# Kernel tuning notes

Measured on AMD Instinct MI355X. Metric: run time of the kernel, lower is better.

Reference implementation:

```python
import jax, jax.numpy as jnp
import numpy as np

N = 100000      # num nodes
E = 1600000     # num edges
B = 256         # num graphs in batch
D_IN = 128
H = 256
BN_EPS = 1e-5


def setup_inputs() -> dict:
    key = jax.random.key(0)
    ks = jax.random.split(key, 16)
    inp = {}
    inp["x"] = jax.random.normal(ks[0], (N, D_IN), jnp.float32)
    inp["edge_index"] = jax.random.randint(ks[1], (2, E), 0, N, jnp.int32)
    inp["edge_weight"] = jax.random.uniform(ks[2], (E,), jnp.float32)
    inp["batch"] = jnp.sort(jax.random.randint(ks[3], (N,), 0, B, jnp.int32))
    # GCN layer 1
    inp["W1"] = jax.random.normal(ks[4], (D_IN, H), jnp.float32) * 0.05
    inp["b1"] = jnp.zeros((H,), jnp.float32)
    inp["g1"] = jnp.ones((H,), jnp.float32)
    inp["be1"] = jnp.zeros((H,), jnp.float32)
    inp["rm1"] = jnp.zeros((H,), jnp.float32)
    inp["rv1"] = jnp.ones((H,), jnp.float32)
    # GCN layer 2
    inp["W2"] = jax.random.normal(ks[5], (H, H), jnp.float32) * 0.05
    inp["b2"] = jnp.zeros((H,), jnp.float32)
    inp["g2"] = jnp.ones((H,), jnp.float32)
    inp["be2"] = jnp.zeros((H,), jnp.float32)
    inp["rm2"] = jnp.zeros((H,), jnp.float32)
    inp["rv2"] = jnp.ones((H,), jnp.float32)
    # classifier: Linear(256,256)+BN, Linear(256,128)+BN, Linear(128,2)
    inp["cW1"] = jax.random.normal(ks[6], (H, 256), jnp.float32) * 0.05
    inp["cb1"] = jnp.zeros((256,), jnp.float32)
    inp["cg1"] = jnp.ones((256,), jnp.float32)
    inp["cbe1"] = jnp.zeros((256,), jnp.float32)
    inp["crm1"] = jnp.zeros((256,), jnp.float32)
    inp["crv1"] = jnp.ones((256,), jnp.float32)
    inp["cW2"] = jax.random.normal(ks[7], (256, 128), jnp.float32) * 0.05
    inp["cb2"] = jnp.zeros((128,), jnp.float32)
    inp["cg2"] = jnp.ones((128,), jnp.float32)
    inp["cbe2"] = jnp.zeros((128,), jnp.float32)
    inp["crm2"] = jnp.zeros((128,), jnp.float32)
    inp["crv2"] = jnp.ones((128,), jnp.float32)
    inp["cW3"] = jax.random.normal(ks[8], (128, 2), jnp.float32) * 0.05
    inp["cb3"] = jnp.zeros((2,), jnp.float32)
    return inp


def _bn(x, g, b, rm, rv):
    # eval-mode BatchNorm1d with running stats
    return (x - rm) * jax.lax.rsqrt(rv + BN_EPS) * g + b


def _gcn_conv(x, W, b, src, dst, ew):
    # PyG GCNConv: add self-loops (weight 1), symmetric normalization
    deg = jax.ops.segment_sum(ew, dst, num_segments=N) + 1.0  # incl. self loop
    dinv = jnp.where(deg > 0, jax.lax.rsqrt(deg), 0.0)        # [N]
    h = x @ W                                                  # [N, out]
    norm = dinv[src] * ew * dinv[dst]                          # [E]
    agg = jax.ops.segment_sum(h[src] * norm[:, None], dst, num_segments=N)
    agg = agg + h * (dinv * dinv)[:, None]                     # self-loop term
    return agg + b


def _forward(x, edge_index, edge_weight, batch,
             W1, b1, g1, be1, rm1, rv1,
             W2, b2, g2, be2, rm2, rv2,
             cW1, cb1, cg1, cbe1, crm1, crv1,
             cW2, cb2, cg2, cbe2, crm2, crv2,
             cW3, cb3):
    src, dst = edge_index[0], edge_index[1]
    # layer 0 (no residual: i == 0)
    h = jax.nn.relu(_bn(_gcn_conv(x, W1, b1, src, dst, edge_weight), g1, be1, rm1, rv1))
    res = h
    # layer 1 (residual: dims match, i > 0); dropout = identity (eval)
    h = jax.nn.relu(_bn(_gcn_conv(h, W2, b2, src, dst, edge_weight), g2, be2, rm2, rv2))
    h = h + res
    # global mean pool per graph
    cnt = jax.ops.segment_sum(jnp.ones((N,), x.dtype), batch, num_segments=B)
    emb = jax.ops.segment_sum(h, batch, num_segments=B) / jnp.maximum(cnt, 1.0)[:, None]
    # classifier MLP
    z = jax.nn.relu(_bn(emb @ cW1 + cb1, cg1, cbe1, crm1, crv1))
    z = jax.nn.relu(_bn(z @ cW2 + cb2, cg2, cbe2, crm2, crv2))
    logits = z @ cW3 + cb3
    return logits, emb


def reference(x, edge_index, edge_weight, batch,
              W1, b1, g1, be1, rm1, rv1,
              W2, b2, g2, be2, rm2, rv2,
              cW1, cb1, cg1, cbe1, crm1, crv1,
              cW2, cb2, cg2, cbe2, crm2, crv2,
              cW3, cb3):
    return _forward(x, edge_index, edge_weight, batch,
                    W1, b1, g1, be1, rm1, rv1,
                    W2, b2, g2, be2, rm2, rv2,
                    cW1, cb1, cg1, cbe1, crm1, crv1,
                    cW2, cb2, cg2, cbe2, crm2, crv2,
                    cW3, cb3)
```

## Files before the change

kernel.cpp:

```cpp
#include <hip/hip_runtime.h>
#include <stdint.h>

#define NN 100000
#define NE 1600000
#define NB 256
#define DIN 128
#define HH 256
#define BN_EPS 1e-5f

typedef unsigned short bf16_t;
typedef __attribute__((ext_vector_type(8))) short short8;
typedef __attribute__((ext_vector_type(4))) short short4v;
typedef __attribute__((ext_vector_type(4))) float f32x4;
typedef __attribute__((ext_vector_type(2))) float f32x2;

struct __align__(8) EPair { int c; float v; };

#define DEG_MASK ((1ULL << 40) - 1ULL)
#define DEG_ONE  (1ULL << 40)
#define FXS 1048576.0f

__device__ __forceinline__ float bf2f(unsigned short u) {
    union { unsigned int i; float f; } v;
    v.i = ((unsigned int)u) << 16;
    return v.f;
}
__device__ __forceinline__ bf16_t f2bf(float f) {
    union { float f; unsigned int i; } v;
    v.f = f;
    unsigned int x = v.i;
    return (bf16_t)((x + 0x7fffu + ((x >> 16) & 1u)) >> 16);
}
__device__ __forceinline__ float ldp(const void* b, int i, int f) {
    return f ? ((const float*)b)[i] : bf2f(((const unsigned short*)b)[i]);
}
__device__ __forceinline__ int dflag_from(const void* rv) {
    return ((((const unsigned int*)rv)[0] & 0xffffu) == 0u) ? 1 : 0;
}

__device__ __forceinline__ void fmadd_row8p(f32x2* acc2, uint2 w, float v) {
#if defined(__HIP_DEVICE_COMPILE__)
    f32x2 vv = {v, v};
    acc2[0] += __builtin_amdgcn_cvt_pk_f32_fp8((int)w.x, false) * vv;
    acc2[1] += __builtin_amdgcn_cvt_pk_f32_fp8((int)w.x, true)  * vv;
    acc2[2] += __builtin_amdgcn_cvt_pk_f32_fp8((int)w.y, false) * vv;
    acc2[3] += __builtin_amdgcn_cvt_pk_f32_fp8((int)w.y, true)  * vv;
#else
    (void)acc2; (void)w; (void)v;
#endif
}
__device__ __forceinline__ unsigned char enc_fp8(float v) {
#if defined(__HIP_DEVICE_COMPILE__)
    int pk = __builtin_amdgcn_cvt_pk_fp8_f32(v, v, 0, false);
    return (unsigned char)(pk & 0xff);
#else
    (void)v; return 0;
#endif
}
__device__ __forceinline__ unsigned int pack4_fp8(float a, float b, float c, float d) {
#if defined(__HIP_DEVICE_COMPILE__)
    int w = __builtin_amdgcn_cvt_pk_fp8_f32(a, b, 0, false);
    w = __builtin_amdgcn_cvt_pk_fp8_f32(c, d, w, true);
    return (unsigned int)w;
#else
    (void)a; (void)b; (void)c; (void)d; return 0;
#endif
}

__device__ __forceinline__ void pack_one(const void* __restrict__ W, bf16_t* __restrict__ P,
                                         int S, int idx, int f) {
    int lane = idx & 63;
    int ts = idx >> 6;
    int s = ts % S;
    int t = ts / S;
    int q = lane >> 4, m = lane & 15;
    int colbase = t * 16 + m;
    int krow = 32 * s + 8 * q;
#pragma unroll
    for (int j = 0; j < 8; j++) P[idx * 8 + j] = f2bf(ldp(W, (krow + j) * 256 + colbase, f));
}

__global__ __launch_bounds__(256) void prep_kernel(const void* __restrict__ x, unsigned int* __restrict__ xc8,
                                                   const void* __restrict__ ew,
                                                   const int* __restrict__ dst,
                                                   const int* __restrict__ batch,
                                                   unsigned long long* __restrict__ cd8,
                                                   unsigned char* __restrict__ occ,
                                                   int* __restrict__ gcount,
                                                   const void* __restrict__ W1, bf16_t* __restrict__ P1,
                                                   const void* __restrict__ W2, bf16_t* __restrict__ P2,
                                                   const void* __restrict__ rv) {
    int i = blockIdx.x * blockDim.x + threadIdx.x;
    int stride = gridDim.x * blockDim.x;
    int shard = blockIdx.x & 7;
    int f = dflag_from(rv);
    if (i < 12288) {
        if (i < 4096) pack_one(W1, P1, 4, i, f);
        else          pack_one(W2, P2, 8, i - 4096, f);
    }
    if (f) {
        const float4* xs = (const float4*)x;
        for (int j = i; j < NN * DIN / 4; j += stride) {
            float4 w = xs[j];
            xc8[j] = pack4_fp8(w.x, w.y, w.z, w.w);
        }
    } else {
        const uint2* xs = (const uint2*)x;
        for (int j = i; j < NN * DIN / 4; j += stride) {
            uint2 w = xs[j];
            xc8[j] = pack4_fp8(bf2f((unsigned short)(w.x & 0xffffu)), bf2f((unsigned short)(w.x >> 16)),
                               bf2f((unsigned short)(w.y & 0xffffu)), bf2f((unsigned short)(w.y >> 16)));
        }
    }
    for (int j = i; j < NE; j += stride) {
        float w = ldp(ew, j, f);
        int d = dst[j];
        unsigned long long wfx = (unsigned long long)(unsigned int)(w * FXS + 0.5f);
        unsigned long long old = atomicAdd(&cd8[(size_t)shard * NN + d], DEG_ONE | wfx);
        occ[j] = (unsigned char)(old >> 40);
    }
    int lane = threadIdx.x & 63;
    for (int j = i; j < NN; j += stride) {
        int b = batch[j];
        bool boundary = (lane == 0) || (j == 0) || (batch[j - 1] != b);
        unsigned long long bmask = __ballot(boundary);
        bool islast = (lane == 63) || (j + 1 >= NN) || (batch[j + 1] != b);
        if (islast) {
            unsigned long long below = bmask & ((lane == 63) ? ~0ull : ((1ull << (lane + 1)) - 1ull));
            int first = 63 - __builtin_clzll(below);
            atomicAdd(&gcount[b], lane - first + 1);
        }
    }
}

#define SCAN_NB ((NN + 1023) / 1024)

__global__ __launch_bounds__(1024) void scanA(const unsigned long long* __restrict__ cd8,
                                              int* __restrict__ rowptr,
                                              float* __restrict__ dinv,
                                              int* __restrict__ bsum) {
    __shared__ int wsum[16];
    int tid = threadIdx.x, lane = tid & 63, wid = tid >> 6;
    int i = blockIdx.x * 1024 + tid;
    int v = 0;
    if (i < NN) {
        float wf = 0.f;
#pragma unroll
        for (int k = 0; k < 8; k++) {
            unsigned long long cv = cd8[(size_t)k * NN + i];
            v += (int)(cv >> 40);
            wf += (float)(cv & DEG_MASK);
        }
        dinv[i] = rsqrtf(wf * (1.0f / FXS) + 1.0f);
    }
    int sc = v;
#pragma unroll
    for (int off = 1; off < 64; off <<= 1) {
        int t = __shfl_up(sc, off, 64);
        if (lane >= off) sc += t;
    }
    if (lane == 63) wsum[wid] = sc;
    __syncthreads();
    if (wid == 0 && lane < 16) {
        int ws = wsum[lane];
        int scw = ws;
#pragma unroll
        for (int off = 1; off < 16; off <<= 1) {
            int t = __shfl_up(scw, off, 64);
            if (lane >= off) scw += t;
        }
        if (lane == 15) bsum[blockIdx.x] = scw;
        wsum[lane] = scw - ws;
    }
    __syncthreads();
    if (i < NN) rowptr[i] = wsum[wid] + sc - v;
}

__global__ __launch_bounds__(64) void scanB(int* __restrict__ bsum, int* __restrict__ rowptr,
                                            const int* __restrict__ gcount, int* __restrict__ gptr,
                                            EPair* __restrict__ ep) {
    int lane = threadIdx.x;
    EPair pz; pz.c = 0; pz.v = 0.f;
    ep[NE + lane] = pz;
    {
        int i0 = lane * 2;
        int v0 = (i0 < SCAN_NB) ? bsum[i0] : 0;
        int v1 = (i0 + 1 < SCAN_NB) ? bsum[i0 + 1] : 0;
        int tsum = v0 + v1;
        int sc = tsum;
#pragma unroll
        for (int off = 1; off < 64; off <<= 1) {
            int t = __shfl_up(sc, off, 64);
            if (lane >= off) sc += t;
        }
        int excl = sc - tsum;
        if (i0 < SCAN_NB) bsum[i0] = excl;
        if (i0 + 1 < SCAN_NB) bsum[i0 + 1] = excl + v0;
        if (lane == 63) rowptr[NN] = sc;
    }
    {
        int i0 = lane * 4;
        int v0 = gcount[i0], v1 = gcount[i0 + 1], v2 = gcount[i0 + 2], v3 = gcount[i0 + 3];
        int tsum = v0 + v1 + v2 + v3;
        int sc = tsum;
#pragma unroll
        for (int off = 1; off < 64; off <<= 1) {
            int t = __shfl_up(sc, off, 64);
            if (lane >= off) sc += t;
        }
        int excl = sc - tsum;
        gptr[i0] = excl;
        gptr[i0 + 1] = excl + v0;
        gptr[i0 + 2] = excl + v0 + v1;
        gptr[i0 + 3] = excl + v0 + v1 + v2;
        if (lane == 63) gptr[256] = sc;
    }
}

__global__ __launch_bounds__(1024) void scanC(int* __restrict__ rowptr, const int* __restrict__ bsum,
                                              const unsigned long long* __restrict__ cd8,
                                              int* __restrict__ offs) {
    int i = blockIdx.x * 1024 + threadIdx.x;
    if (i < NN) {
        int rp = rowptr[i] + bsum[blockIdx.x];
        rowptr[i] = rp;
        int cum = rp;
#pragma unroll
        for (int k = 0; k < 8; k++) {
            offs[(size_t)k * NN + i] = cum;
            cum += (int)(cd8[(size_t)k * NN + i] >> 40);
        }
    }
}

__global__ __launch_bounds__(256) void scatter_kernel(const int* __restrict__ src,
                                                      const int* __restrict__ dst,
                                                      const void* __restrict__ ew,
                                                      const float* __restrict__ dinv,
                                                      const int* __restrict__ offs,
                                                      const unsigned char* __restrict__ occ,
                                                      EPair* __restrict__ ep,
                                                      const void* __restrict__ rv) {
    int i = blockIdx.x * blockDim.x + threadIdx.x;
    int f = dflag_from(rv);
    int shard = blockIdx.x & 7;
    if (i < NE) {
        int s = src[i], d = dst[i];
        float nv = dinv[s] * ldp(ew, i, f) * dinv[d];
        int pos = offs[(size_t)shard * NN + d] + occ[i];
        EPair pr;
        pr.c = s;
        pr.v = nv;
        ep[pos] = pr;
    }
}

template <int K, bool WRITE_OUT, bool ACCUM>
__global__ __launch_bounds__(256, 6) void fused_layer(
        const void* __restrict__ Xv,
        const bf16_t* __restrict__ P,
        const int* __restrict__ rowptr,
        const EPair* __restrict__ ep,
        const float* __restrict__ dinv,
        const int* __restrict__ batch,
        const void* __restrict__ bias,
        const void* __restrict__ gam,
        const void* __restrict__ bet,
        const void* __restrict__ rmean,
        const void* __restrict__ rvar,
        void* __restrict__ outbuf,
        float* __restrict__ partial,
        float* __restrict__ partial2,
        float* __restrict__ embf) {
    constexpr int S = K / 32;
    constexpr int ROWELL = K + 8;
    constexpr int LPR = K / 8;
    constexpr int EDG = 64 / LPR;
    constexpr int UN = 8;
    constexpr int BE = EDG * UN;
    constexpr int U16 = 16 / EDG;
    constexpr int U32 = 32 / EDG;
    constexpr int SH = (K == 256) ? 8 : 7;
    __shared__ __align__(16) bf16_t T[16 * ROWELL];
    __shared__ EPair WINDOW[4][64];
    const char* Xb = (const char*)Xv;
    int fl = dflag_from(rvar);
    int widx = threadIdx.x >> 6;
    int lane = threadIdx.x & 63;
    int h = lane / LPR;
    int l = lane % LPR;
    int f0 = l * 8;
    unsigned loff = (unsigned)(l * 8);
    int rowbase = blockIdx.x * 16;

    int rp = rowptr[rowbase + (lane < 17 ? lane : 16)];
    float dvv = dinv[rowbase + (lane < 16 ? lane : 15)];

    int j0 = widx * 4;
    EPair win = ep[__shfl(rp, j0) + lane];
    for (int j = 0; j < 4; j++) {
        int r = j0 + j;
        int e0 = __shfl(rp, r);
        int e1 = __shfl(rp, r + 1);
        int n = e1 - e0;
        float di = __shfl(dvv, r);
        int node = rowbase + r;
        EPair nxtwin = ep[e1 + lane];
        f32x2 acc2[4];
#pragma unroll
        for (int c = 0; c < 4; c++) acc2[c] = (f32x2){0.f, 0.f};
        {
            EPair sw;
            bool okl = lane < n;
            sw.c = okl ? win.c : node;
            sw.v = okl ? win.v : 0.f;
            WINDOW[widx][lane] = sw;
        }
        uint2 wself = *(const uint2*)(Xb + ((unsigned)node << SH) + loff);

#define GBATCH(B0, NU) { \
        uint2 wreg[NU]; \
        float vreg[NU]; \
        _Pragma("unroll") \
        for (int u = 0; u < NU; u++) { \
            EPair e = WINDOW[widx][(B0) + EDG * u + h]; \
            vreg[u] = e.v; \
            wreg[u] = *(const uint2*)(Xb + ((unsigned)e.c << SH) + loff); \
        } \
        _Pragma("unroll") \
        for (int u = 0; u < NU; u++) fmadd_row8p(acc2, wreg[u], vreg[u]); \
    }

        if (n <= 16) {
            GBATCH(0, U16)
        } else if (n <= 32) {
            GBATCH(0, U32)
        } else {
            int base = 0;
            while (true) {
                int winend = n - base;
                if (winend > 64) winend = 64;
                for (int s0 = 0; s0 < winend; s0 += BE) {
                    GBATCH(s0, UN)
                }
                base += winend;
                if (base >= n) break;
                EPair nw = ep[e0 + base + lane];
                EPair sw;
                bool okl = (base + lane) < n;
                sw.c = okl ? nw.c : node;
                sw.v = okl ? nw.v : 0.f;
                WINDOW[widx][lane] = sw;
            }
        }
#undef GBATCH
        fmadd_row8p(acc2, wself, (h == 0) ? di * di : 0.f);
        float acc[8];
#pragma unroll
        for (int c = 0; c < 4; c++) { acc[2 * c] = acc2[c][0]; acc[2 * c + 1] = acc2[c][1]; }
#pragma unroll
        for (int d = LPR; d < 64; d <<= 1) {
#pragma unroll
            for (int c = 0; c < 8; c++) acc[c] += __shfl_xor(acc[c], d);
        }
        if (h == 0) {
            short8 o;
#pragma unroll
            for (int c = 0; c < 8; c++) o[c] = (short)f2bf(acc[c]);
            *(short8*)&T[r * ROWELL + f0] = o;
        }
        win = nxtwin;
    }
    __syncthreads();

    int m = lane & 15, q = lane >> 4;
    f32x4 acc16[4];
#pragma unroll
    for (int tt = 0; tt < 4; tt++) acc16[tt] = (f32x4){0.f, 0.f, 0.f, 0.f};
#pragma unroll
    for (int s = 0; s < S; s++) {
        short8 af = *(const short8*)&T[m * ROWELL + 32 * s + 8 * q];
#pragma unroll
        for (int tt = 0; tt < 4; tt++) {
            int t = j0 + tt;
            short8 bfr = *(const short8*)(P + ((size_t)(t * S + s) * 64 + lane) * 8);
            acc16[tt] = __builtin_amdgcn_mfma_f32_16x16x32_bf16(af, bfr, acc16[tt], 0, 0, 0);
        }
    }
    if (WRITE_OUT) __syncthreads();
    unsigned char* T8 = (unsigned char*)T;

    int g0 = batch[rowbase];
    int g15 = batch[rowbase + 15];
    int rg[4];
#pragma unroll
    for (int r = 0; r < 4; r++) rg[r] = batch[rowbase + q * 4 + r];
#pragma unroll
    for (int tt = 0; tt < 4; tt++) {
        int col = (j0 + tt) * 16 + m;
        float a = rsqrtf(ldp(rvar, col, fl) + BN_EPS) * ldp(gam, col, fl);
        float bc = (ldp(bias, col, fl) - ldp(rmean, col, fl)) * a + ldp(bet, col, fl);
        float cs0 = 0.f, cs1 = 0.f;
#pragma unroll
        for (int r = 0; r < 4; r++) {
            int row = q * 4 + r;
            float v = fmaxf(acc16[tt][r] * a + bc, 0.f);
            if (WRITE_OUT) T8[row * 256 + col] = enc_fp8(v);
            if (rg[r] == g0) cs0 += v;
            else if (rg[r] == g15) cs1 += v;
            else atomicAdd(&embf[(size_t)rg[r] * 256 + col], v);
        }
        cs0 += __shfl_xor(cs0, 16, 64);
        cs0 += __shfl_xor(cs0, 32, 64);
        cs1 += __shfl_xor(cs1, 16, 64);
        cs1 += __shfl_xor(cs1, 32, 64);
        if (q == 0) {
            size_t pidx = (size_t)blockIdx.x * 256 + col;
            partial[pidx]  = (ACCUM ? partial[pidx]  : 0.f) + cs0;
            partial2[pidx] = (ACCUM ? partial2[pidx] : 0.f) + cs1;
        }
    }
    if (WRITE_OUT) {
        __syncthreads();
        int tid = threadIdx.x;
        uint4 wv = *(const uint4*)&T8[tid * 16];
        *(uint4*)((char*)outbuf + (size_t)rowbase * 256 + tid * 16) = wv;
    }
}

__global__ __launch_bounds__(256) void classifier_kernel(const float* __restrict__ partial,
                                                         const float* __restrict__ partial2,
                                                         const int* __restrict__ gptr,
                                                         const float* __restrict__ embf,
                                                         const void* cW1, const void* cb1,
                                                         const void* cg1, const void* cbe1,
                                                         const void* crm1, const void* crv1,
                                                         const void* cW2, const void* cb2,
                                                         const void* cg2, const void* cbe2,
                                                         const void* crm2, const void* crv2,
                                                         const void* cW3, const void* cb3,
                                                         void* __restrict__ d_out) {
    int g = blockIdx.x, tid = threadIdx.x;
    int fl = dflag_from(crv1);
    __shared__ float se[256];
    __shared__ float z1[256];
    __shared__ float z2[128];
    int s = gptr[g], e = gptr[g + 1];
    float acc = embf[g * 256 + tid];
    int blo = (s + 15) >> 4, bhi = (e + 15) >> 4;
    for (int b = blo; b < bhi; b++) acc += partial[(size_t)b * 256 + tid];
    int bs = s >> 4;
    if ((s & 15) && (16 * bs + 15) < e) acc += partial2[(size_t)bs * 256 + tid];
    float mval = acc / fmaxf((float)(e - s), 1.f);
    se[tid] = mval;
    if (fl) ((float*)d_out)[512 + g * 256 + tid] = mval;
    else    ((bf16_t*)d_out)[512 + g * 256 + tid] = f2bf(mval);
    __syncthreads();
    {
        float sm = 0.f;
#pragma unroll 8
        for (int k = 0; k < 256; k++) sm += se[k] * ldp(cW1, k * 256 + tid, fl);
        sm += ldp(cb1, tid, fl);
        sm = (sm - ldp(crm1, tid, fl)) * rsqrtf(ldp(crv1, tid, fl) + BN_EPS) * ldp(cg1, tid, fl) + ldp(cbe1, tid, fl);
        z1[tid] = fmaxf(sm, 0.f);
    }
    __syncthreads();
    if (tid < 128) {
        float sm = 0.f;
#pragma unroll 8
        for (int k = 0; k < 256; k++) sm += z1[k] * ldp(cW2, k * 128 + tid, fl);
        sm += ldp(cb2, tid, fl);
        sm = (sm - ldp(crm2, tid, fl)) * rsqrtf(ldp(crv2, tid, fl) + BN_EPS) * ldp(cg2, tid, fl) + ldp(cbe2, tid, fl);
        z2[tid] = fmaxf(sm, 0.f);
    }
    __syncthreads();
    if (tid < 2) {
        float sm = 0.f;
        for (int k = 0; k < 128; k++) sm += z2[k] * ldp(cW3, k * 2 + tid, fl);
        sm += ldp(cb3, tid, fl);
        if (fl) ((float*)d_out)[g * 2 + tid] = sm;
        else    ((bf16_t*)d_out)[g * 2 + tid] = f2bf(sm);
    }
}

extern "C" void kernel_launch(void* const* d_in, const int* in_sizes, int n_in,
                              void* d_out, int out_size, void* d_ws, size_t ws_size,
                              hipStream_t stream) {
    const void* x    = d_in[0];
    const int*  eidx = (const int*)d_in[1];
    const void* ew   = d_in[2];
    const int*  batch= (const int*)d_in[3];
    const void* W1   = d_in[4];
    const void* b1   = d_in[5];
    const void* g1   = d_in[6];
    const void* be1  = d_in[7];
    const void* rm1  = d_in[8];
    const void* rv1  = d_in[9];
    const void* W2   = d_in[10];
    const void* b2   = d_in[11];
    const void* g2   = d_in[12];
    const void* be2  = d_in[13];
    const void* rm2  = d_in[14];
    const void* rv2  = d_in[15];
    const void* cW1  = d_in[16];
    const void* cb1  = d_in[17];
    const void* cg1  = d_in[18];
    const void* cbe1 = d_in[19];
    const void* crm1 = d_in[20];
    const void* crv1 = d_in[21];
    const void* cW2  = d_in[22];
    const void* cb2  = d_in[23];
    const void* cg2  = d_in[24];
    const void* cbe2 = d_in[25];
    const void* crm2 = d_in[26];
    const void* crv2 = d_in[27];
    const void* cW3  = d_in[28];
    const void* cb3  = d_in[29];

    const int* src = eidx;
    const int* dst = eidx + NE;

    char* p = (char*)d_ws;
    auto alloc = [&](size_t bytes) -> void* {
        void* r = (void*)p;
        p += (bytes + 255) & ~(size_t)255;
        return r;
    };
    unsigned long long* cd8 = (unsigned long long*)alloc((size_t)8 * NN * 8);
    int*    gcount = (int*)alloc((size_t)NB * 4);
    float*  embf   = (float*)alloc((size_t)NB * 256 * 4);
    size_t zspan = (char*)p - (char*)cd8;
    int*    rowptr = (int*)alloc((size_t)(NN + 1) * 4);
    float*  dinv   = (float*)alloc((size_t)NN * 4);
    int*    bsum   = (int*)alloc((size_t)SCAN_NB * 4);
    int*    gptr   = (int*)alloc((size_t)(NB + 1) * 4);
    int*    offs   = (int*)alloc((size_t)8 * NN * 4);
    unsigned char* occ = (unsigned char*)alloc((size_t)NE);
    float*  partial = (float*)alloc((size_t)(NN / 16) * 256 * 4);
    float*  partial2= (float*)alloc((size_t)(NN / 16) * 256 * 4);
    EPair*  ep     = (EPair*)alloc((size_t)(NE + 64) * 8);
    unsigned int* xc8 = (unsigned int*)alloc((size_t)NN * DIN);
    bf16_t* pW1    = (bf16_t*)alloc((size_t)DIN * 256 * 2);
    bf16_t* pW2    = (bf16_t*)alloc((size_t)256 * 256 * 2);
    void*   hl     = alloc((size_t)NN * 256);

    (void)hipMemsetAsync(cd8, 0, zspan, stream);

    prep_kernel<<<2048, 256, 0, stream>>>(x, xc8, ew, dst, batch, cd8, occ, gcount,
                                          W1, pW1, W2, pW2, rv1);
    scanA<<<SCAN_NB, 1024, 0, stream>>>(cd8, rowptr, dinv, bsum);
    scanB<<<1, 64, 0, stream>>>(bsum, rowptr, gcount, gptr, ep);
    scanC<<<SCAN_NB, 1024, 0, stream>>>(rowptr, bsum, cd8, offs);
    scatter_kernel<<<NE / 256, 256, 0, stream>>>(src, dst, ew, dinv, offs, occ, ep, rv1);

    int blocks = NN / 16;
    fused_layer<128, true, false><<<blocks, 256, 0, stream>>>(
        xc8, pW1, rowptr, ep, dinv, batch, b1, g1, be1, rm1, rv1, hl, partial, partial2, embf);
    fused_layer<256, false, true><<<blocks, 256, 0, stream>>>(
        hl, pW2, rowptr, ep, dinv, batch, b2, g2, be2, rm2, rv2, nullptr, partial, partial2, embf);

    classifier_kernel<<<NB, 256, 0, stream>>>(partial, partial2, gptr, embf,
                                              cW1, cb1, cg1, cbe1, crm1, crv1,
                                              cW2, cb2, cg2, cbe2, crm2, crv2,
                                              cW3, cb3, d_out);
}
```

Baseline: 487.5 us.

## Software-pipeline neighbor gathers across rows with double-buffered edge windows

When all four rows a wavefront handles have at most 32 edges, the gather phase now issues the feature loads for the next row before accumulating the current one, using two shared-memory edge windows and two register sets. The aim is to hide global gather latency by keeping more loads in flight per wave. The n<=16 special case is dropped, so short rows always do a full 32-edge batch with padding. The launch bound drops from 6 to 4 waves per SIMD to make room for the extra registers, which lowers occupancy.

```diff
diff --git a/kernel.cpp b/kernel.cpp
--- a/kernel.cpp
+++ b/kernel.cpp
@@ -256,7 +256,7 @@
 }
 
 template <int K, bool WRITE_OUT, bool ACCUM>
-__global__ __launch_bounds__(256, 6) void fused_layer(
+__global__ __launch_bounds__(256, 4) void fused_layer(
         const void* __restrict__ Xv,
         const bf16_t* __restrict__ P,
         const int* __restrict__ rowptr,
@@ -278,11 +278,10 @@
     constexpr int EDG = 64 / LPR;
     constexpr int UN = 8;
     constexpr int BE = EDG * UN;
-    constexpr int U16 = 16 / EDG;
     constexpr int U32 = 32 / EDG;
     constexpr int SH = (K == 256) ? 8 : 7;
     __shared__ __align__(16) bf16_t T[16 * ROWELL];
-    __shared__ EPair WINDOW[4][64];
+    __shared__ EPair WIN2[4][2][64];
     const char* Xb = (const char*)Xv;
     int fl = dflag_from(rvar);
     int widx = threadIdx.x >> 6;
@@ -297,51 +296,109 @@
     float dvv = dinv[rowbase + (lane < 16 ? lane : 15)];
 
     int j0 = widx * 4;
-    EPair win = ep[__shfl(rp, j0) + lane];
-    for (int j = 0; j < 4; j++) {
-        int r = j0 + j;
-        int e0 = __shfl(rp, r);
-        int e1 = __shfl(rp, r + 1);
-        int n = e1 - e0;
-        float di = __shfl(dvv, r);
-        int node = rowbase + r;
-        EPair nxtwin = ep[e1 + lane];
-        f32x2 acc2[4];
-#pragma unroll
-        for (int c = 0; c < 4; c++) acc2[c] = (f32x2){0.f, 0.f};
-        {
-            EPair sw;
-            bool okl = lane < n;
-            sw.c = okl ? win.c : node;
-            sw.v = okl ? win.v : 0.f;
-            WINDOW[widx][lane] = sw;
-        }
-        uint2 wself = *(const uint2*)(Xb + ((unsigned)node << SH) + loff);
-
-#define GBATCH(B0, NU) { \
-        uint2 wreg[NU]; \
-        float vreg[NU]; \
+    int e_0 = __shfl(rp, j0),     e_1 = __shfl(rp, j0 + 1);
+    int e_2 = __shfl(rp, j0 + 2), e_3 = __shfl(rp, j0 + 3);
+    int e_4 = __shfl(rp, j0 + 4);
+    int n0 = e_1 - e_0, n1 = e_2 - e_1, n2 = e_3 - e_2, n3 = e_4 - e_3;
+    float di0 = __shfl(dvv, j0),     di1 = __shfl(dvv, j0 + 1);
+    float di2 = __shfl(dvv, j0 + 2), di3 = __shfl(dvv, j0 + 3);
+    int nd0 = rowbase + j0, nd1 = nd0 + 1, nd2 = nd0 + 2, nd3 = nd0 + 3;
+    int nmax = max(max(n0, n1), max(n2, n3));
+    EPair w_next = ep[e_0 + lane];
+
+#define PSTAGE(SL, NV, ND) { \
+        EPair sw_; bool ok_ = lane < (NV); \
+        sw_.c = ok_ ? w_next.c : (ND); \
+        sw_.v = ok_ ? w_next.v : 0.f; \
+        WIN2[widx][SL][lane] = sw_; }
+
+#define PISSUE(WR, WS, SL, ND) { \
         _Pragma("unroll") \
-        for (int u = 0; u < NU; u++) { \
-            EPair e = WINDOW[widx][(B0) + EDG * u + h]; \
-            vreg[u] = e.v; \
-            wreg[u] = *(const uint2*)(Xb + ((unsigned)e.c << SH) + loff); \
+        for (int u = 0; u < U32; u++) { \
+            int c_ = WIN2[widx][SL][EDG * u + h].c; \
+            WR[u] = *(const uint2*)(Xb + ((unsigned)c_ << SH) + loff); \
         } \
+        WS = *(const uint2*)(Xb + ((unsigned)(ND) << SH) + loff); }
+
+#define PCONSUME(WR, WS, SL, DI, RR) { \
+        f32x2 acc2[4]; \
         _Pragma("unroll") \
-        for (int u = 0; u < NU; u++) fmadd_row8p(acc2, wreg[u], vreg[u]); \
-    }
-
-        if (n <= 16) {
-            GBATCH(0, U16)
-        } else if (n <= 32) {
-            GBATCH(0, U32)
-        } else {
+        for (int c_ = 0; c_ < 4; c_++) acc2[c_] = (f32x2){0.f, 0.f}; \
+        _Pragma("unroll") \
+        for (int u = 0; u < U32; u++) { \
+            float v_ = WIN2[widx][SL][EDG * u + h].v; \
+            fmadd_row8p(acc2, WR[u], v_); \
+        } \
+        fmadd_row8p(acc2, WS, (h == 0) ? (DI) * (DI) : 0.f); \
+        float acc[8]; \
+        _Pragma("unroll") \
+        for (int c_ = 0; c_ < 4; c_++) { acc[2 * c_] = acc2[c_][0]; acc[2 * c_ + 1] = acc2[c_][1]; } \
+        _Pragma("unroll") \
+        for (int d_ = LPR; d_ < 64; d_ <<= 1) { \
+            _Pragma("unroll") \
+            for (int c_ = 0; c_ < 8; c_++) acc[c_] += __shfl_xor(acc[c_], d_); \
+        } \
+        if (h == 0) { \
+            short8 o_; \
+            _Pragma("unroll") \
+            for (int c_ = 0; c_ < 8; c_++) o_[c_] = (short)f2bf(acc[c_]); \
+            *(short8*)&T[(RR) * ROWELL + f0] = o_; \
+        } }
+
+    if (nmax <= 32) {
+        uint2 wregA[U32], wregB[U32];
+        uint2 wselfA, wselfB;
+        PSTAGE(0, n0, nd0)
+        w_next = ep[e_1 + lane];
+        PISSUE(wregA, wselfA, 0, nd0)
+        PSTAGE(1, n1, nd1)
+        w_next = ep[e_2 + lane];
+        PISSUE(wregB, wselfB, 1, nd1)
+        PCONSUME(wregA, wselfA, 0, di0, j0 + 0)
+        PSTAGE(0, n2, nd2)
+        w_next = ep[e_3 + lane];
+        PISSUE(wregA, wselfA, 0, nd2)
+        PCONSUME(wregB, wselfB, 1, di1, j0 + 1)
+        PSTAGE(1, n3, nd3)
+        PISSUE(wregB, wselfB, 1, nd3)
+        PCONSUME(wregA, wselfA, 0, di2, j0 + 2)
+        PCONSUME(wregB, wselfB, 1, di3, j0 + 3)
+    } else {
+        EPair win = w_next;
+        for (int j = 0; j < 4; j++) {
+            int r = j0 + j;
+            int e0 = __shfl(rp, r);
+            int e1 = __shfl(rp, r + 1);
+            int n = e1 - e0;
+            float di = __shfl(dvv, r);
+            int node = rowbase + r;
+            EPair nxtwin = ep[e1 + lane];
+            f32x2 acc2[4];
+#pragma unroll
+            for (int c = 0; c < 4; c++) acc2[c] = (f32x2){0.f, 0.f};
+            {
+                EPair sw;
+                bool okl = lane < n;
+                sw.c = okl ? win.c : node;
+                sw.v = okl ? win.v : 0.f;
+                WIN2[widx][0][lane] = sw;
+            }
+            uint2 wself = *(const uint2*)(Xb + ((unsigned)node << SH) + loff);
             int base = 0;
             while (true) {
                 int winend = n - base;
                 if (winend > 64) winend = 64;
                 for (int s0 = 0; s0 < winend; s0 += BE) {
-                    GBATCH(s0, UN)
+                    uint2 wreg[UN];
+                    float vreg[UN];
+#pragma unroll
+                    for (int u = 0; u < UN; u++) {
+                        EPair e = WIN2[widx][0][s0 + EDG * u + h];
+                        vreg[u] = e.v;
+                        wreg[u] = *(const uint2*)(Xb + ((unsigned)e.c << SH) + loff);
+                    }
+#pragma unroll
+                    for (int u = 0; u < UN; u++) fmadd_row8p(acc2, wreg[u], vreg[u]);
                 }
                 base += winend;
                 if (base >= n) break;
@@ -350,27 +407,29 @@
                 bool okl = (base + lane) < n;
                 sw.c = okl ? nw.c : node;
                 sw.v = okl ? nw.v : 0.f;
-                WINDOW[widx][lane] = sw;
+                WIN2[widx][0][lane] = sw;
             }
-        }
-#undef GBATCH
-        fmadd_row8p(acc2, wself, (h == 0) ? di * di : 0.f);
-        float acc[8];
-#pragma unroll
-        for (int c = 0; c < 4; c++) { acc[2 * c] = acc2[c][0]; acc[2 * c + 1] = acc2[c][1]; }
-#pragma unroll
-        for (int d = LPR; d < 64; d <<= 1) {
-#pragma unroll
-            for (int c = 0; c < 8; c++) acc[c] += __shfl_xor(acc[c], d);
-        }
-        if (h == 0) {
-            short8 o;
-#pragma unroll
-            for (int c = 0; c < 8; c++) o[c] = (short)f2bf(acc[c]);
-            *(short8*)&T[r * ROWELL + f0] = o;
-        }
-        win = nxtwin;
-    }
+            fmadd_row8p(acc2, wself, (h == 0) ? di * di : 0.f);
+            float acc[8];
+#pragma unroll
+            for (int c = 0; c < 4; c++) { acc[2 * c] = acc2[c][0]; acc[2 * c + 1] = acc2[c][1]; }
+#pragma unroll
+            for (int d = LPR; d < 64; d <<= 1) {
+#pragma unroll
+                for (int c = 0; c < 8; c++) acc[c] += __shfl_xor(acc[c], d);
+            }
+            if (h == 0) {
+                short8 o;
+#pragma unroll
+                for (int c = 0; c < 8; c++) o[c] = (short)f2bf(acc[c]);
+                *(short8*)&T[r * ROWELL + f0] = o;
+            }
+            win = nxtwin;
+        }
+    }
+#undef PSTAGE
+#undef PISSUE
+#undef PCONSUME
     __syncthreads();
 
     int m = lane & 15, q = lane >> 4;
```

Result: no change. 497.1 us (+2.0%).
